# Performance work log

Measured on AMD Instinct MI355X. Metric: run time of the kernel, lower is better.

The kernel has to match this reference:

```python
import jax, jax.numpy as jnp
import numpy as np

EPS = 1e-5


def _layer_norm(x, gamma, beta):
    mu = jnp.mean(x, axis=-1, keepdims=True)
    var = jnp.var(x, axis=-1, keepdims=True)
    return (x - mu) * jax.lax.rsqrt(var + EPS) * gamma + beta


def setup_inputs() -> dict:
    key = jax.random.key(0)
    B, I, H = 4096, 1024, 1024
    ks = jax.random.split(key, 6)
    x = jax.random.normal(ks[0], (B, I), dtype=jnp.float32)
    h = jax.random.normal(ks[1], (B, H), dtype=jnp.float32)
    c = jax.random.normal(ks[2], (B, H), dtype=jnp.float32)
    # nn.Linear(I+H, 4H): weight [4H, I+H], bias [4H]
    bound = 1.0 / np.sqrt(I + H)
    W = jax.random.uniform(ks[3], (4 * H, I + H), minval=-bound, maxval=bound, dtype=jnp.float32)
    b = jax.random.uniform(ks[4], (4 * H,), minval=-bound, maxval=bound, dtype=jnp.float32)
    inp = {"x": x, "h": h, "c": c, "W": W, "b": b}
    for name in ("i", "f", "g", "o", "c"):
        inp[f"ln_{name}_g"] = jnp.ones((H,), dtype=jnp.float32)
        inp[f"ln_{name}_b"] = jnp.zeros((H,), dtype=jnp.float32)
    return inp


def reference(x, h, c, W, b, ln_i_g, ln_i_b, ln_f_g, ln_f_b, ln_g_g, ln_g_b,
              ln_o_g, ln_o_b, ln_c_g, ln_c_b):
    H = h.shape[-1]
    xh = jnp.concatenate([x, h], axis=-1)              # [B, I+H]
    gates = xh @ W.T + b                               # [B, 4H]
    i_raw, f_raw, g_raw, o_raw = jnp.split(gates, 4, axis=-1)
    i = jax.nn.sigmoid(_layer_norm(i_raw, ln_i_g, ln_i_b))
    f = jax.nn.sigmoid(_layer_norm(f_raw, ln_f_g, ln_f_b))
    g = jnp.tanh(_layer_norm(g_raw, ln_g_g, ln_g_b))
    o = jax.nn.sigmoid(_layer_norm(o_raw, ln_o_g, ln_o_b))
    c_new = f * c + i * g
    h_new = o * jnp.tanh(_layer_norm(c_new, ln_c_g, ln_c_b))
    return (h_new, c_new)
```

## Files before the change

kernel.cpp:

```cpp
#include <hip/hip_runtime.h>
#include <hip/hip_bf16.h>

#define B_ROWS 4096
#define H_DIM  1024
#define K_DIM  2048
#define N_DIM  4096
#define NT32   64

typedef __attribute__((ext_vector_type(8))) short bf16x8;
typedef __attribute__((ext_vector_type(4))) float f32x4;

__device__ __forceinline__ unsigned short f2bf(float f) {
  union { float f; unsigned int u; } v; v.f = f;
  unsigned int u = v.u;
  return (unsigned short)((u + 0x7fffu + ((u >> 16) & 1u)) >> 16);
}
__device__ __forceinline__ float bf2f(unsigned short u) {
  union { unsigned int u; float f; } v; v.u = ((unsigned int)u) << 16;
  return v.f;
}

__device__ __forceinline__ void gload_lds16(const void* g, void* l) {
  __builtin_amdgcn_global_load_lds(
      (const __attribute__((address_space(1))) void*)g,
      (__attribute__((address_space(3))) void*)l, 16, 0, 0);
}

__global__ __launch_bounds__(256) void pack_kernel(
    const float* __restrict__ x, const float* __restrict__ h,
    const float* __restrict__ W, unsigned short* __restrict__ Abf,
    unsigned short* __restrict__ Wbf) {
  int bid = blockIdx.x;
  if (bid < 8192) {
    int t = bid * 256 + threadIdx.x;
    int e = t * 4;
    int row = e >> 11;
    int col = e & 2047;
    const float* src = (col < 1024) ? (x + (size_t)row * 1024 + col)
                                    : (h + (size_t)row * 1024 + (col - 1024));
    float4 v = *(const float4*)src;
    ushort4 o;
    o.x = f2bf(v.x); o.y = f2bf(v.y); o.z = f2bf(v.z); o.w = f2bf(v.w);
    *(ushort4*)(Abf + e) = o;
  } else {
    int t = (bid - 8192) * 256 + threadIdx.x;
    int e = t * 4;
    float4 v = *(const float4*)(W + e);
    ushort4 o;
    o.x = f2bf(v.x); o.y = f2bf(v.y); o.z = f2bf(v.z); o.w = f2bf(v.w);
    *(ushort4*)(Wbf + e) = o;
  }
}


#define UNR _Pragma("unroll")

#define TILE1(tt, BUF, FRa, FRb, FWa, FWb)                                   \
  {                                                                          \
    const int kt3 = ((tt) + 3) & (NT32 - 1);                                 \
    char* const Ld = lds + (((BUF) + 3) & 3) * 32768;                        \
    const unsigned short* pA = gAw + ((size_t)kt3 << 5);                     \
    const unsigned short* pB = gBw + ((size_t)kt3 << 5);                     \
    gload_lds16(pA, Ld + dstOfs);                                            \
    gload_lds16(pA + 16 * K_DIM, Ld + dstOfs + 1024);                        \
    gload_lds16(pB, Ld + 16384 + dstOfs);                                    \
    gload_lds16(pB + 16 * K_DIM, Ld + 16384 + dstOfs + 1024);                \
    asm volatile("s_waitcnt vmcnt(8)" ::: "memory");                         \
    __builtin_amdgcn_s_barrier();                                            \
    const char* const Ln = lds + (((BUF) + 1) & 3) * 32768;                  \
    UNR for (int mi = 0; mi < 8; ++mi)                                       \
      FWa[mi] = *(const bf16x8*)(Ln + (wm * 8 + mi) * 1024 + lofs);          \
    UNR for (int ni = 0; ni < 4; ++ni)                                       \
      FWb[ni] = *(const bf16x8*)(Ln + 16384 + (wn * 4 + ni) * 1024 + lofs);  \
    asm volatile("s_waitcnt lgkmcnt(12)" ::: "memory");                      \
    __builtin_amdgcn_sched_barrier(0);                                       \
    __builtin_amdgcn_s_setprio(1);                                           \
    UNR for (int mi = 0; mi < 8; ++mi)                                       \
      UNR for (int ni = 0; ni < 4; ++ni)                                     \
        acc[mi][ni] = __builtin_amdgcn_mfma_f32_16x16x32_bf16(               \
            FRa[mi], FRb[ni], acc[mi][ni], 0, 0, 0);                         \
    __builtin_amdgcn_s_setprio(0);                                           \
  }

#define PSTAGE(kt, BUFOFS)                                                   \
  {                                                                          \
    const unsigned short* pA = gAw + ((size_t)(kt) << 5);                    \
    const unsigned short* pB = gBw + ((size_t)(kt) << 5);                    \
    char* const Ld = lds + (BUFOFS);                                         \
    gload_lds16(pA, Ld + dstOfs);                                            \
    gload_lds16(pA + 16 * K_DIM, Ld + dstOfs + 1024);                        \
    gload_lds16(pB, Ld + 16384 + dstOfs);                                    \
    gload_lds16(pB + 16 * K_DIM, Ld + 16384 + dstOfs + 1024);                \
  }

__global__ __launch_bounds__(512, 2) void gemm_kernel(
    const unsigned short* __restrict__ A, const unsigned short* __restrict__ W,
    const float* __restrict__ bias, unsigned short* __restrict__ C) {
  __shared__ __align__(16) char lds[131072];

  const int tid = threadIdx.x;
  const int w = tid >> 6, l = tid & 63;
  const int wm = w >> 2, wn = w & 3;

  const int bid = blockIdx.x;
  const int xcd = bid & 7, li = bid >> 3;
  const int by = (xcd & 3) * 4 + (li >> 3);
  const int bx = ((xcd >> 2) << 3) + (li & 7);
  const int bm = by * 256, bn = bx * 256;

  const int lofs = (((l & 15) * 64) + ((l >> 4) * 16)) ^ ((l & 8) << 2);
  const int lane_r = (l >> 2) & 15;
  const int lane_c = ((l & 3) * 8) ^ (((l >> 5) & 1) * 16);

  const int dstOfs = w * 2048;
  const unsigned short* gAw = A + (size_t)(bm + 32 * w + lane_r) * K_DIM + lane_c;
  const unsigned short* gBw = W + (size_t)(bn + 32 * w + lane_r) * K_DIM + lane_c;

  f32x4 acc[8][4];
#pragma unroll
  for (int i = 0; i < 8; ++i)
#pragma unroll
    for (int j = 0; j < 4; ++j) acc[i][j] = (f32x4)0.0f;

  PSTAGE(0, 0);
  PSTAGE(1, 32768);
  PSTAGE(2, 65536);
  asm volatile("s_waitcnt vmcnt(8)" ::: "memory");
  __builtin_amdgcn_s_barrier();

  bf16x8 aP[8], bP[4], aQ[8], bQ[4];
#pragma unroll
  for (int mi = 0; mi < 8; ++mi)
    aP[mi] = *(const bf16x8*)(lds + (wm * 8 + mi) * 1024 + lofs);
#pragma unroll
  for (int ni = 0; ni < 4; ++ni)
    bP[ni] = *(const bf16x8*)(lds + 16384 + (wn * 4 + ni) * 1024 + lofs);

  for (int t = 0; t < NT32; t += 4) {
    TILE1(t + 0, 0, aP, bP, aQ, bQ);
    TILE1(t + 1, 1, aQ, bQ, aP, bP);
    TILE1(t + 2, 2, aP, bP, aQ, bQ);
    TILE1(t + 3, 3, aQ, bQ, aP, bP);
  }

  const int lm = l & 15, lq = l >> 4;
  float bv[4];
#pragma unroll
  for (int ni = 0; ni < 4; ++ni) bv[ni] = bias[bn + wn * 64 + ni * 16 + lm];
  unsigned short* Cb = C + (size_t)(bm + wm * 128) * N_DIM + bn + wn * 64;
#pragma unroll
  for (int mi = 0; mi < 8; ++mi)
#pragma unroll
    for (int j = 0; j < 4; ++j) {
      const size_t rofs = (size_t)(mi * 16 + lq * 4 + j) * N_DIM;
#pragma unroll
      for (int ni = 0; ni < 4; ++ni)
        Cb[rofs + ni * 16 + lm] = f2bf(acc[mi][ni][j] + bv[ni]);
    }
}

__device__ __forceinline__ float2 blk_sum2(float s, float q, float* red,
                                           int wid, int lane) {
#pragma unroll
  for (int o = 32; o >= 1; o >>= 1) {
    s += __shfl_xor(s, o, 64);
    q += __shfl_xor(q, o, 64);
  }
  __syncthreads();
  if (lane == 0) { red[wid * 2] = s; red[wid * 2 + 1] = q; }
  __syncthreads();
  s = red[0] + red[2] + red[4] + red[6];
  q = red[1] + red[3] + red[5] + red[7];
  return make_float2(s, q);
}

__device__ __forceinline__ float sigmoidf_(float x) {
  return 1.0f / (1.0f + __expf(-x));
}
__device__ __forceinline__ float tanhf_(float x) {
  return 1.0f - 2.0f / (__expf(2.0f * x) + 1.0f);
}

__global__ __launch_bounds__(256) void ln_lstm_kernel(
    const unsigned short* __restrict__ gates, const float* __restrict__ cprev,
    const float* __restrict__ g_i, const float* __restrict__ b_i,
    const float* __restrict__ g_f, const float* __restrict__ b_f,
    const float* __restrict__ g_g, const float* __restrict__ b_g,
    const float* __restrict__ g_o, const float* __restrict__ b_o,
    const float* __restrict__ g_c, const float* __restrict__ b_c,
    float* __restrict__ out) {
  const int b = blockIdx.x;
  const int t = threadIdx.x;
  const int wid = t >> 6, lane = t & 63;
  __shared__ float red[8];

  const unsigned short* grow = gates + (size_t)b * N_DIM;
  const int c0 = t * 4;

  float v[4][4];
#pragma unroll
  for (int g = 0; g < 4; g++) {
    ushort4 raw = *(const ushort4*)(grow + g * 1024 + c0);
    v[g][0] = bf2f(raw.x); v[g][1] = bf2f(raw.y);
    v[g][2] = bf2f(raw.z); v[g][3] = bf2f(raw.w);
  }

  const float4 gamma[4] = {*(const float4*)(g_i + c0), *(const float4*)(g_f + c0),
                           *(const float4*)(g_g + c0), *(const float4*)(g_o + c0)};
  const float4 beta[4]  = {*(const float4*)(b_i + c0), *(const float4*)(b_f + c0),
                           *(const float4*)(b_g + c0), *(const float4*)(b_o + c0)};

  float a[4][4];
#pragma unroll
  for (int g = 0; g < 4; g++) {
    float s = v[g][0] + v[g][1] + v[g][2] + v[g][3];
    float q = v[g][0]*v[g][0] + v[g][1]*v[g][1] + v[g][2]*v[g][2] + v[g][3]*v[g][3];
    float2 r = blk_sum2(s, q, red, wid, lane);
    float mu = r.x * (1.0f / 1024.0f);
    float var = r.y * (1.0f / 1024.0f) - mu * mu;
    float inv = rsqrtf(var + 1e-5f);
    const float* gm = (const float*)&gamma[g];
    const float* bt = (const float*)&beta[g];
#pragma unroll
    for (int j = 0; j < 4; j++) {
      float n = (v[g][j] - mu) * inv * gm[j] + bt[j];
      a[g][j] = (g == 2) ? tanhf_(n) : sigmoidf_(n);
    }
  }

  float4 cp = *(const float4*)(cprev + (size_t)b * 1024 + c0);
  const float* cpe = (const float*)&cp;
  float cn[4];
#pragma unroll
  for (int j = 0; j < 4; j++)
    cn[j] = a[1][j] * cpe[j] + a[0][j] * a[2][j];

  {
    float s = cn[0] + cn[1] + cn[2] + cn[3];
    float q = cn[0]*cn[0] + cn[1]*cn[1] + cn[2]*cn[2] + cn[3]*cn[3];
    float2 r = blk_sum2(s, q, red, wid, lane);
    float mu = r.x * (1.0f / 1024.0f);
    float var = r.y * (1.0f / 1024.0f) - mu * mu;
    float inv = rsqrtf(var + 1e-5f);
    float4 gm = *(const float4*)(g_c + c0);
    float4 bt = *(const float4*)(b_c + c0);
    const float* gme = (const float*)&gm;
    const float* bte = (const float*)&bt;
    float hn[4];
#pragma unroll
    for (int j = 0; j < 4; j++) {
      float n = (cn[j] - mu) * inv * gme[j] + bte[j];
      hn[j] = a[3][j] * tanhf_(n);
    }
    *(float4*)(out + (size_t)b * 1024 + c0) = make_float4(hn[0], hn[1], hn[2], hn[3]);
    *(float4*)(out + (size_t)B_ROWS * H_DIM + (size_t)b * 1024 + c0) =
        make_float4(cn[0], cn[1], cn[2], cn[3]);
  }
}

extern "C" void kernel_launch(void* const* d_in, const int* in_sizes, int n_in,
                              void* d_out, int out_size, void* d_ws,
                              size_t ws_size, hipStream_t stream) {
  const float* x    = (const float*)d_in[0];
  const float* h    = (const float*)d_in[1];
  const float* c    = (const float*)d_in[2];
  const float* W    = (const float*)d_in[3];
  const float* bias = (const float*)d_in[4];
  const float* ln_i_g = (const float*)d_in[5];
  const float* ln_i_b = (const float*)d_in[6];
  const float* ln_f_g = (const float*)d_in[7];
  const float* ln_f_b = (const float*)d_in[8];
  const float* ln_g_g = (const float*)d_in[9];
  const float* ln_g_b = (const float*)d_in[10];
  const float* ln_o_g = (const float*)d_in[11];
  const float* ln_o_b = (const float*)d_in[12];
  const float* ln_c_g = (const float*)d_in[13];
  const float* ln_c_b = (const float*)d_in[14];

  unsigned short* Abf = (unsigned short*)d_ws;
  unsigned short* Wbf = Abf + (size_t)B_ROWS * K_DIM;
  unsigned short* gates = Wbf + (size_t)N_DIM * K_DIM;

  pack_kernel<<<16384, 256, 0, stream>>>(x, h, W, Abf, Wbf);

  dim3 ggrid(256);
  gemm_kernel<<<ggrid, 512, 0, stream>>>(Abf, Wbf, bias, gates);

  ln_lstm_kernel<<<B_ROWS, 256, 0, stream>>>(
      gates, c, ln_i_g, ln_i_b, ln_f_g, ln_f_b, ln_g_g, ln_g_b,
      ln_o_g, ln_o_b, ln_c_g, ln_c_b, (float*)d_out);
}
```

Before: 105.3 us.

## Shrink GEMM tile to 256x128 with 4 waves and triple-buffered LDS

The GEMM moves from a 256x256 tile with 8 waves and a 4-stage LDS ring to a 256x128 tile with 4 waves and a 3-stage ring, launching 512 blocks instead of 256. Each wave still computes a 128x64 sub-tile, and it now issues 6 global-to-LDS loads per stage. The prefetch distance drops from 3 tiles ahead to 2, and the XCD-to-block mapping is rearranged for the new grid shape. The smaller LDS footprint should let more blocks fit per CU and fill all CUs better, at the cost of more global traffic per FLOP from the narrower N tile and less latency hiding.

Result: slower. 117.6 us (+11.7%).

```diff
diff --git a/kernel.cpp b/kernel.cpp
--- a/kernel.cpp
+++ b/kernel.cpp
@@ -55,23 +55,27 @@
 
 #define UNR _Pragma("unroll")
 
-#define TILE1(tt, BUF, FRa, FRb, FWa, FWb)                                   \
+#define PSTG(kt, BS)                                                         \
   {                                                                          \
-    const int kt3 = ((tt) + 3) & (NT32 - 1);                                 \
-    char* const Ld = lds + (((BUF) + 3) & 3) * 32768;                        \
-    const unsigned short* pA = gAw + ((size_t)kt3 << 5);                     \
-    const unsigned short* pB = gBw + ((size_t)kt3 << 5);                     \
-    gload_lds16(pA, Ld + dstOfs);                                            \
-    gload_lds16(pA + 16 * K_DIM, Ld + dstOfs + 1024);                        \
-    gload_lds16(pB, Ld + 16384 + dstOfs);                                    \
-    gload_lds16(pB + 16 * K_DIM, Ld + 16384 + dstOfs + 1024);                \
-    asm volatile("s_waitcnt vmcnt(8)" ::: "memory");                         \
+    const unsigned short* pA = gAw + ((size_t)(kt) << 5);                    \
+    const unsigned short* pB = gBw + ((size_t)(kt) << 5);                    \
+    UNR for (int i = 0; i < 4; ++i)                                          \
+      gload_lds16(pA + (size_t)i * 16 * K_DIM, (BS) + (4 * w + i) * 1024);   \
+    UNR for (int i = 0; i < 2; ++i)                                          \
+      gload_lds16(pB + (size_t)i * 16 * K_DIM,                               \
+                  (BS) + 16384 + (2 * w + i) * 1024);                        \
+  }
+
+#define TILE(tt, BS, BR, FRa, FRb, FWa, FWb)                                 \
+  {                                                                          \
+    const int kt2 = ((tt) + 2) & (NT32 - 1);                                 \
+    PSTG(kt2, BS);                                                           \
+    asm volatile("s_waitcnt vmcnt(6)" ::: "memory");                         \
     __builtin_amdgcn_s_barrier();                                            \
-    const char* const Ln = lds + (((BUF) + 1) & 3) * 32768;                  \
     UNR for (int mi = 0; mi < 8; ++mi)                                       \
-      FWa[mi] = *(const bf16x8*)(Ln + (wm * 8 + mi) * 1024 + lofs);          \
+      FWa[mi] = *(const bf16x8*)((BR) + (wm * 8 + mi) * 1024 + lofs);        \
     UNR for (int ni = 0; ni < 4; ++ni)                                       \
-      FWb[ni] = *(const bf16x8*)(Ln + 16384 + (wn * 4 + ni) * 1024 + lofs);  \
+      FWb[ni] = *(const bf16x8*)((BR) + 16384 + (wn * 4 + ni) * 1024 + lofs);\
     asm volatile("s_waitcnt lgkmcnt(12)" ::: "memory");                      \
     __builtin_amdgcn_sched_barrier(0);                                       \
     __builtin_amdgcn_s_setprio(1);                                           \
@@ -82,66 +86,64 @@
     __builtin_amdgcn_s_setprio(0);                                           \
   }
 
-#define PSTAGE(kt, BUFOFS)                                                   \
-  {                                                                          \
-    const unsigned short* pA = gAw + ((size_t)(kt) << 5);                    \
-    const unsigned short* pB = gBw + ((size_t)(kt) << 5);                    \
-    char* const Ld = lds + (BUFOFS);                                         \
-    gload_lds16(pA, Ld + dstOfs);                                            \
-    gload_lds16(pA + 16 * K_DIM, Ld + dstOfs + 1024);                        \
-    gload_lds16(pB, Ld + 16384 + dstOfs);                                    \
-    gload_lds16(pB + 16 * K_DIM, Ld + 16384 + dstOfs + 1024);                \
-  }
-
-__global__ __launch_bounds__(512, 2) void gemm_kernel(
+__global__ __launch_bounds__(256, 2) void gemm_kernel(
     const unsigned short* __restrict__ A, const unsigned short* __restrict__ W,
     const float* __restrict__ bias, unsigned short* __restrict__ C) {
-  __shared__ __align__(16) char lds[131072];
+  __shared__ __align__(16) char lds[73728];
 
   const int tid = threadIdx.x;
   const int w = tid >> 6, l = tid & 63;
-  const int wm = w >> 2, wn = w & 3;
+  const int wm = w >> 1, wn = w & 1;
 
   const int bid = blockIdx.x;
   const int xcd = bid & 7, li = bid >> 3;
-  const int by = (xcd & 3) * 4 + (li >> 3);
-  const int bx = ((xcd >> 2) << 3) + (li & 7);
-  const int bm = by * 256, bn = bx * 256;
+  const int by = (xcd & 1) * 8 + (li >> 3);
+  const int bx = ((xcd >> 1) << 3) + (li & 7);
+  const int bm = by * 256, bn = bx * 128;
 
   const int lofs = (((l & 15) * 64) + ((l >> 4) * 16)) ^ ((l & 8) << 2);
   const int lane_r = (l >> 2) & 15;
   const int lane_c = ((l & 3) * 8) ^ (((l >> 5) & 1) * 16);
 
-  const int dstOfs = w * 2048;
-  const unsigned short* gAw = A + (size_t)(bm + 32 * w + lane_r) * K_DIM + lane_c;
+  const unsigned short* gAw = A + (size_t)(bm + 64 * w + lane_r) * K_DIM + lane_c;
   const unsigned short* gBw = W + (size_t)(bn + 32 * w + lane_r) * K_DIM + lane_c;
 
+  char* const LB0 = lds;
+  char* const LB1 = lds + 24576;
+  char* const LB2 = lds + 49152;
+
   f32x4 acc[8][4];
 #pragma unroll
   for (int i = 0; i < 8; ++i)
 #pragma unroll
     for (int j = 0; j < 4; ++j) acc[i][j] = (f32x4)0.0f;
 
-  PSTAGE(0, 0);
-  PSTAGE(1, 32768);
-  PSTAGE(2, 65536);
-  asm volatile("s_waitcnt vmcnt(8)" ::: "memory");
+  PSTG(0, LB0);
+  PSTG(1, LB1);
+  asm volatile("s_waitcnt vmcnt(6)" ::: "memory");
   __builtin_amdgcn_s_barrier();
 
   bf16x8 aP[8], bP[4], aQ[8], bQ[4];
 #pragma unroll
   for (int mi = 0; mi < 8; ++mi)
-    aP[mi] = *(const bf16x8*)(lds + (wm * 8 + mi) * 1024 + lofs);
+    aP[mi] = *(const bf16x8*)(LB0 + (wm * 8 + mi) * 1024 + lofs);
 #pragma unroll
   for (int ni = 0; ni < 4; ++ni)
-    bP[ni] = *(const bf16x8*)(lds + 16384 + (wn * 4 + ni) * 1024 + lofs);
-
-  for (int t = 0; t < NT32; t += 4) {
-    TILE1(t + 0, 0, aP, bP, aQ, bQ);
-    TILE1(t + 1, 1, aQ, bQ, aP, bP);
-    TILE1(t + 2, 2, aP, bP, aQ, bQ);
-    TILE1(t + 3, 3, aQ, bQ, aP, bP);
-  }
+    bP[ni] = *(const bf16x8*)(LB0 + 16384 + (wn * 4 + ni) * 1024 + lofs);
+
+  for (int i = 0; i < 10; ++i) {
+    const int t = i * 6;
+    TILE(t + 0, LB2, LB1, aP, bP, aQ, bQ);
+    TILE(t + 1, LB0, LB2, aQ, bQ, aP, bP);
+    TILE(t + 2, LB1, LB0, aP, bP, aQ, bQ);
+    TILE(t + 3, LB2, LB1, aQ, bQ, aP, bP);
+    TILE(t + 4, LB0, LB2, aP, bP, aQ, bQ);
+    TILE(t + 5, LB1, LB0, aQ, bQ, aP, bP);
+  }
+  TILE(60, LB2, LB1, aP, bP, aQ, bQ);
+  TILE(61, LB0, LB2, aQ, bQ, aP, bP);
+  TILE(62, LB1, LB0, aP, bP, aQ, bQ);
+  TILE(63, LB2, LB1, aQ, bQ, aP, bP);
 
   const int lm = l & 15, lq = l >> 4;
   float bv[4];
@@ -283,8 +285,8 @@
 
   pack_kernel<<<16384, 256, 0, stream>>>(x, h, W, Abf, Wbf);
 
-  dim3 ggrid(256);
-  gemm_kernel<<<ggrid, 512, 0, stream>>>(Abf, Wbf, bias, gates);
+  dim3 ggrid(512);
+  gemm_kernel<<<ggrid, 256, 0, stream>>>(Abf, Wbf, bias, gates);
 
   ln_lstm_kernel<<<B_ROWS, 256, 0, stream>>>(
       gates, c, ln_i_g, ln_i_b, ln_f_g, ln_f_b, ln_g_g, ln_g_b,
```

## Switch GEMM to 32x32x16 MFMA tiles and batch LayerNorm gate reductions

Applied to the files above, without the earlier changes.

The GEMM inner loop moves from 16x16x32 MFMA to 32x32x16 bf16 MFMA with 4x2 accumulator tiles per wave. This changes the LDS fragment addressing, the global-to-LDS lane mapping and the epilogue store pattern. The larger instruction is meant to cut LDS fragment reads and instruction issue per unit of math. The LN-LSTM kernel also reduces all four gate sums and sums of squares in one pass with a single barrier, instead of four separate block reductions. The new swizzled addressing risks bank conflicts or layout errors if it does not match the load mapping.

Measured after the change: 111.0 us. 5.5% more time.

```diff
diff --git a/kernel.cpp b/kernel.cpp
--- a/kernel.cpp
+++ b/kernel.cpp
@@ -8,7 +8,7 @@
 #define NT32   64
 
 typedef __attribute__((ext_vector_type(8))) short bf16x8;
-typedef __attribute__((ext_vector_type(4))) float f32x4;
+typedef __attribute__((ext_vector_type(16))) float f32x16;
 
 __device__ __forceinline__ unsigned short f2bf(float f) {
   union { float f; unsigned int u; } v; v.f = f;
@@ -55,42 +55,42 @@
 
 #define UNR _Pragma("unroll")
 
+#define PSTG(kt, BUFOFS)                                                     \
+  {                                                                          \
+    const size_t ko = (size_t)(kt) << 5;                                     \
+    char* const Ld = lds + (BUFOFS);                                         \
+    gload_lds16(gAw0 + ko, Ld + dstOfs);                                     \
+    gload_lds16(gAw1 + ko, Ld + dstOfs + 1024);                              \
+    gload_lds16(gBw0 + ko, Ld + 16384 + dstOfs);                             \
+    gload_lds16(gBw1 + ko, Ld + 16384 + dstOfs + 1024);                      \
+  }
+
 #define TILE1(tt, BUF, FRa, FRb, FWa, FWb)                                   \
   {                                                                          \
     const int kt3 = ((tt) + 3) & (NT32 - 1);                                 \
-    char* const Ld = lds + (((BUF) + 3) & 3) * 32768;                        \
-    const unsigned short* pA = gAw + ((size_t)kt3 << 5);                     \
-    const unsigned short* pB = gBw + ((size_t)kt3 << 5);                     \
-    gload_lds16(pA, Ld + dstOfs);                                            \
-    gload_lds16(pA + 16 * K_DIM, Ld + dstOfs + 1024);                        \
-    gload_lds16(pB, Ld + 16384 + dstOfs);                                    \
-    gload_lds16(pB + 16 * K_DIM, Ld + 16384 + dstOfs + 1024);                \
+    PSTG(kt3, (((BUF) + 3) & 3) * 32768);                                    \
     asm volatile("s_waitcnt vmcnt(8)" ::: "memory");                         \
     __builtin_amdgcn_s_barrier();                                            \
     const char* const Ln = lds + (((BUF) + 1) & 3) * 32768;                  \
-    UNR for (int mi = 0; mi < 8; ++mi)                                       \
-      FWa[mi] = *(const bf16x8*)(Ln + (wm * 8 + mi) * 1024 + lofs);          \
-    UNR for (int ni = 0; ni < 4; ++ni)                                       \
-      FWb[ni] = *(const bf16x8*)(Ln + 16384 + (wn * 4 + ni) * 1024 + lofs);  \
+    UNR for (int R = 0; R < 4; ++R) {                                        \
+      FWa[R][0] = *(const bf16x8*)(Ln + (wm * 8 + 2 * R) * 1024 + lofs0);    \
+      FWa[R][1] = *(const bf16x8*)(Ln + (wm * 8 + 2 * R) * 1024 + lofs1);    \
+    }                                                                        \
+    UNR for (int ni = 0; ni < 2; ++ni) {                                     \
+      FWb[ni][0] = *(const bf16x8*)(Ln + 16384 +                             \
+                                    (wn * 4 + 2 * ni) * 1024 + lofs0);       \
+      FWb[ni][1] = *(const bf16x8*)(Ln + 16384 +                             \
+                                    (wn * 4 + 2 * ni) * 1024 + lofs1);       \
+    }                                                                        \
     asm volatile("s_waitcnt lgkmcnt(12)" ::: "memory");                      \
     __builtin_amdgcn_sched_barrier(0);                                       \
     __builtin_amdgcn_s_setprio(1);                                           \
-    UNR for (int mi = 0; mi < 8; ++mi)                                       \
-      UNR for (int ni = 0; ni < 4; ++ni)                                     \
-        acc[mi][ni] = __builtin_amdgcn_mfma_f32_16x16x32_bf16(               \
-            FRa[mi], FRb[ni], acc[mi][ni], 0, 0, 0);                         \
+    UNR for (int R = 0; R < 4; ++R)                                          \
+      UNR for (int ni = 0; ni < 2; ++ni)                                     \
+        UNR for (int h = 0; h < 2; ++h)                                      \
+          acc[R][ni] = __builtin_amdgcn_mfma_f32_32x32x16_bf16(              \
+              FRa[R][h], FRb[ni][h], acc[R][ni], 0, 0, 0);                   \
     __builtin_amdgcn_s_setprio(0);                                           \
-  }
-
-#define PSTAGE(kt, BUFOFS)                                                   \
-  {                                                                          \
-    const unsigned short* pA = gAw + ((size_t)(kt) << 5);                    \
-    const unsigned short* pB = gBw + ((size_t)(kt) << 5);                    \
-    char* const Ld = lds + (BUFOFS);                                         \
-    gload_lds16(pA, Ld + dstOfs);                                            \
-    gload_lds16(pA + 16 * K_DIM, Ld + dstOfs + 1024);                        \
-    gload_lds16(pB, Ld + 16384 + dstOfs);                                    \
-    gload_lds16(pB + 16 * K_DIM, Ld + 16384 + dstOfs + 1024);                \
   }
 
 __global__ __launch_bounds__(512, 2) void gemm_kernel(
@@ -108,33 +108,43 @@
   const int bx = ((xcd >> 2) << 3) + (li & 7);
   const int bm = by * 256, bn = bx * 256;
 
-  const int lofs = (((l & 15) * 64) + ((l >> 4) * 16)) ^ ((l & 8) << 2);
+  const int lofs0 = ((l >> 4) & 1) * 1024 + (l & 15) * 64 +
+                    ((((l >> 5) * 16) ^ ((l & 8) << 2)) ^ (((l >> 4) & 1) << 4));
+  const int lofs1 = lofs0 ^ 32;
+
   const int lane_r = (l >> 2) & 15;
-  const int lane_c = ((l & 3) * 8) ^ (((l >> 5) & 1) * 16);
+  const int lane_c0 = ((l & 3) * 8) ^ (((l >> 5) & 1) * 16);
+  const int lane_c1 = lane_c0 ^ 8;
 
   const int dstOfs = w * 2048;
-  const unsigned short* gAw = A + (size_t)(bm + 32 * w + lane_r) * K_DIM + lane_c;
-  const unsigned short* gBw = W + (size_t)(bn + 32 * w + lane_r) * K_DIM + lane_c;
-
-  f32x4 acc[8][4];
-#pragma unroll
-  for (int i = 0; i < 8; ++i)
-#pragma unroll
-    for (int j = 0; j < 4; ++j) acc[i][j] = (f32x4)0.0f;
-
-  PSTAGE(0, 0);
-  PSTAGE(1, 32768);
-  PSTAGE(2, 65536);
+  const unsigned short* gAw0 = A + (size_t)(bm + 32 * w + lane_r) * K_DIM + lane_c0;
+  const unsigned short* gAw1 = A + (size_t)(bm + 32 * w + 16 + lane_r) * K_DIM + lane_c1;
+  const unsigned short* gBw0 = W + (size_t)(bn + 32 * w + lane_r) * K_DIM + lane_c0;
+  const unsigned short* gBw1 = W + (size_t)(bn + 32 * w + 16 + lane_r) * K_DIM + lane_c1;
+
+  f32x16 acc[4][2];
+#pragma unroll
+  for (int i = 0; i < 4; ++i)
+#pragma unroll
+    for (int j = 0; j < 2; ++j) acc[i][j] = (f32x16)0.0f;
+
+  PSTG(0, 0);
+  PSTG(1, 32768);
+  PSTG(2, 65536);
   asm volatile("s_waitcnt vmcnt(8)" ::: "memory");
   __builtin_amdgcn_s_barrier();
 
-  bf16x8 aP[8], bP[4], aQ[8], bQ[4];
-#pragma unroll
-  for (int mi = 0; mi < 8; ++mi)
-    aP[mi] = *(const bf16x8*)(lds + (wm * 8 + mi) * 1024 + lofs);
-#pragma unroll
-  for (int ni = 0; ni < 4; ++ni)
-    bP[ni] = *(const bf16x8*)(lds + 16384 + (wn * 4 + ni) * 1024 + lofs);
+  bf16x8 aP[4][2], bP[2][2], aQ[4][2], bQ[2][2];
+#pragma unroll
+  for (int R = 0; R < 4; ++R) {
+    aP[R][0] = *(const bf16x8*)(lds + (wm * 8 + 2 * R) * 1024 + lofs0);
+    aP[R][1] = *(const bf16x8*)(lds + (wm * 8 + 2 * R) * 1024 + lofs1);
+  }
+#pragma unroll
+  for (int ni = 0; ni < 2; ++ni) {
+    bP[ni][0] = *(const bf16x8*)(lds + 16384 + (wn * 4 + 2 * ni) * 1024 + lofs0);
+    bP[ni][1] = *(const bf16x8*)(lds + 16384 + (wn * 4 + 2 * ni) * 1024 + lofs1);
+  }
 
   for (int t = 0; t < NT32; t += 4) {
     TILE1(t + 0, 0, aP, bP, aQ, bQ);
@@ -143,35 +153,20 @@
     TILE1(t + 3, 3, aQ, bQ, aP, bP);
   }
 
-  const int lm = l & 15, lq = l >> 4;
-  float bv[4];
-#pragma unroll
-  for (int ni = 0; ni < 4; ++ni) bv[ni] = bias[bn + wn * 64 + ni * 16 + lm];
+  const int cl = l & 31, hi = l >> 5;
+  float bv[2];
+#pragma unroll
+  for (int ni = 0; ni < 2; ++ni) bv[ni] = bias[bn + wn * 64 + ni * 32 + cl];
   unsigned short* Cb = C + (size_t)(bm + wm * 128) * N_DIM + bn + wn * 64;
 #pragma unroll
-  for (int mi = 0; mi < 8; ++mi)
-#pragma unroll
-    for (int j = 0; j < 4; ++j) {
-      const size_t rofs = (size_t)(mi * 16 + lq * 4 + j) * N_DIM;
-#pragma unroll
-      for (int ni = 0; ni < 4; ++ni)
-        Cb[rofs + ni * 16 + lm] = f2bf(acc[mi][ni][j] + bv[ni]);
-    }
-}
-
-__device__ __forceinline__ float2 blk_sum2(float s, float q, float* red,
-                                           int wid, int lane) {
-#pragma unroll
-  for (int o = 32; o >= 1; o >>= 1) {
-    s += __shfl_xor(s, o, 64);
-    q += __shfl_xor(q, o, 64);
-  }
-  __syncthreads();
-  if (lane == 0) { red[wid * 2] = s; red[wid * 2 + 1] = q; }
-  __syncthreads();
-  s = red[0] + red[2] + red[4] + red[6];
-  q = red[1] + red[3] + red[5] + red[7];
-  return make_float2(s, q);
+  for (int R = 0; R < 4; ++R)
+#pragma unroll
+    for (int ni = 0; ni < 2; ++ni)
+#pragma unroll
+      for (int r = 0; r < 16; ++r) {
+        const int row = R * 32 + (r & 3) + 8 * (r >> 2) + 4 * hi;
+        Cb[(size_t)row * N_DIM + ni * 32 + cl] = f2bf(acc[R][ni][r] + bv[ni]);
+      }
 }
 
 __device__ __forceinline__ float sigmoidf_(float x) {
@@ -192,7 +187,7 @@
   const int b = blockIdx.x;
   const int t = threadIdx.x;
   const int wid = t >> 6, lane = t & 63;
-  __shared__ float red[8];
+  __shared__ float red[32];
 
   const unsigned short* grow = gates + (size_t)b * N_DIM;
   const int c0 = t * 4;
@@ -210,14 +205,29 @@
   const float4 beta[4]  = {*(const float4*)(b_i + c0), *(const float4*)(b_f + c0),
                            *(const float4*)(b_g + c0), *(const float4*)(b_o + c0)};
 
+  float s[8];
+#pragma unroll
+  for (int g = 0; g < 4; g++) {
+    s[g]     = v[g][0] + v[g][1] + v[g][2] + v[g][3];
+    s[4 + g] = v[g][0]*v[g][0] + v[g][1]*v[g][1] + v[g][2]*v[g][2] + v[g][3]*v[g][3];
+  }
+#pragma unroll
+  for (int o = 32; o >= 1; o >>= 1)
+#pragma unroll
+    for (int i = 0; i < 8; i++) s[i] += __shfl_xor(s[i], o, 64);
+  if (lane == 0) {
+#pragma unroll
+    for (int i = 0; i < 8; i++) red[wid * 8 + i] = s[i];
+  }
+  __syncthreads();
+#pragma unroll
+  for (int i = 0; i < 8; i++) s[i] = red[i] + red[8 + i] + red[16 + i] + red[24 + i];
+
   float a[4][4];
 #pragma unroll
   for (int g = 0; g < 4; g++) {
-    float s = v[g][0] + v[g][1] + v[g][2] + v[g][3];
-    float q = v[g][0]*v[g][0] + v[g][1]*v[g][1] + v[g][2]*v[g][2] + v[g][3]*v[g][3];
-    float2 r = blk_sum2(s, q, red, wid, lane);
-    float mu = r.x * (1.0f / 1024.0f);
-    float var = r.y * (1.0f / 1024.0f) - mu * mu;
+    float mu = s[g] * (1.0f / 1024.0f);
+    float var = s[4 + g] * (1.0f / 1024.0f) - mu * mu;
     float inv = rsqrtf(var + 1e-5f);
     const float* gm = (const float*)&gamma[g];
     const float* bt = (const float*)&beta[g];
@@ -236,11 +246,20 @@
     cn[j] = a[1][j] * cpe[j] + a[0][j] * a[2][j];
 
   {
-    float s = cn[0] + cn[1] + cn[2] + cn[3];
-    float q = cn[0]*cn[0] + cn[1]*cn[1] + cn[2]*cn[2] + cn[3]*cn[3];
-    float2 r = blk_sum2(s, q, red, wid, lane);
-    float mu = r.x * (1.0f / 1024.0f);
-    float var = r.y * (1.0f / 1024.0f) - mu * mu;
+    float u0 = cn[0] + cn[1] + cn[2] + cn[3];
+    float u1 = cn[0]*cn[0] + cn[1]*cn[1] + cn[2]*cn[2] + cn[3]*cn[3];
+#pragma unroll
+    for (int o = 32; o >= 1; o >>= 1) {
+      u0 += __shfl_xor(u0, o, 64);
+      u1 += __shfl_xor(u1, o, 64);
+    }
+    __syncthreads();
+    if (lane == 0) { red[wid * 2] = u0; red[wid * 2 + 1] = u1; }
+    __syncthreads();
+    u0 = red[0] + red[2] + red[4] + red[6];
+    u1 = red[1] + red[3] + red[5] + red[7];
+    float mu = u0 * (1.0f / 1024.0f);
+    float var = u1 * (1.0f / 1024.0f) - mu * mu;
     float inv = rsqrtf(var + 1e-5f);
     float4 gm = *(const float4*)(g_c + c0);
     float4 bt = *(const float4*)(b_c + c0);
```

## Fuse pack, GEMM and LayerNorm-LSTM into one cooperative kernel with grid syncs

Applied to the files above, without the earlier changes.

Merges the three launches (bf16 pack, MFMA GEMM, LN-LSTM epilogue) into a single cooperative kernel of 256 blocks, separated by grid-wide syncs. This removes two kernel launch gaps and the tail of each stage. The LN stage is rewritten so each wave handles a whole row and reduces with shuffles only, instead of a block-wide LDS reduction. The GEMM inner tile also changes its waits and adds sched_group_barrier interleaving of MFMA and LDS reads. In exchange, the pack and LN stages now run with only 256 blocks of 512 threads, which lowers their occupancy and parallelism, and the grid syncs add their own overhead.

Result: slower. 185.5 us (+76.2%).

```diff
diff --git a/kernel.cpp b/kernel.cpp
--- a/kernel.cpp
+++ b/kernel.cpp
@@ -1,5 +1,8 @@
 #include <hip/hip_runtime.h>
 #include <hip/hip_bf16.h>
+#include <hip/hip_cooperative_groups.h>
+
+namespace cg = cooperative_groups;
 
 #define B_ROWS 4096
 #define H_DIM  1024
@@ -26,267 +29,281 @@
       (__attribute__((address_space(3))) void*)l, 16, 0, 0);
 }
 
-__global__ __launch_bounds__(256) void pack_kernel(
-    const float* __restrict__ x, const float* __restrict__ h,
-    const float* __restrict__ W, unsigned short* __restrict__ Abf,
-    unsigned short* __restrict__ Wbf) {
-  int bid = blockIdx.x;
-  if (bid < 8192) {
-    int t = bid * 256 + threadIdx.x;
-    int e = t * 4;
-    int row = e >> 11;
-    int col = e & 2047;
-    const float* src = (col < 1024) ? (x + (size_t)row * 1024 + col)
-                                    : (h + (size_t)row * 1024 + (col - 1024));
-    float4 v = *(const float4*)src;
-    ushort4 o;
-    o.x = f2bf(v.x); o.y = f2bf(v.y); o.z = f2bf(v.z); o.w = f2bf(v.w);
-    *(ushort4*)(Abf + e) = o;
-  } else {
-    int t = (bid - 8192) * 256 + threadIdx.x;
-    int e = t * 4;
-    float4 v = *(const float4*)(W + e);
-    ushort4 o;
-    o.x = f2bf(v.x); o.y = f2bf(v.y); o.z = f2bf(v.z); o.w = f2bf(v.w);
-    *(ushort4*)(Wbf + e) = o;
-  }
-}
-
+__device__ __forceinline__ float sigmoidf_(float x) {
+  return 1.0f / (1.0f + __expf(-x));
+}
+__device__ __forceinline__ float tanhf_(float x) {
+  return 1.0f - 2.0f / (__expf(2.0f * x) + 1.0f);
+}
+
+struct KParams {
+  const float *x, *h, *c, *W, *bias;
+  const float *gi, *bi2, *gf, *bf2, *gg, *bg2, *go, *bo2, *gc, *bc2;
+  unsigned short *Abf, *Wbf, *gates;
+  float *out;
+};
 
 #define UNR _Pragma("unroll")
+
+#define PSTG(kt, BUFOFS)                                                     \
+  {                                                                          \
+    const size_t ko = (size_t)(kt) << 5;                                     \
+    char* const Ld = lds + (BUFOFS);                                         \
+    gload_lds16(gAw + ko, Ld + dstOfs);                                      \
+    gload_lds16(gAw + ko + 16 * K_DIM, Ld + dstOfs + 1024);                  \
+    gload_lds16(gBw + ko, Ld + 16384 + dstOfs);                              \
+    gload_lds16(gBw + ko + 16 * K_DIM, Ld + 16384 + dstOfs + 1024);          \
+  }
 
 #define TILE1(tt, BUF, FRa, FRb, FWa, FWb)                                   \
   {                                                                          \
     const int kt3 = ((tt) + 3) & (NT32 - 1);                                 \
-    char* const Ld = lds + (((BUF) + 3) & 3) * 32768;                        \
-    const unsigned short* pA = gAw + ((size_t)kt3 << 5);                     \
-    const unsigned short* pB = gBw + ((size_t)kt3 << 5);                     \
-    gload_lds16(pA, Ld + dstOfs);                                            \
-    gload_lds16(pA + 16 * K_DIM, Ld + dstOfs + 1024);                        \
-    gload_lds16(pB, Ld + 16384 + dstOfs);                                    \
-    gload_lds16(pB + 16 * K_DIM, Ld + 16384 + dstOfs + 1024);                \
+    PSTG(kt3, (((BUF) + 3) & 3) * 32768);                                    \
     asm volatile("s_waitcnt vmcnt(8)" ::: "memory");                         \
     __builtin_amdgcn_s_barrier();                                            \
+    asm volatile("s_waitcnt lgkmcnt(0)" ::: "memory");                       \
+    __builtin_amdgcn_sched_barrier(0);                                       \
     const char* const Ln = lds + (((BUF) + 1) & 3) * 32768;                  \
+    __builtin_amdgcn_s_setprio(1);                                           \
     UNR for (int mi = 0; mi < 8; ++mi)                                       \
       FWa[mi] = *(const bf16x8*)(Ln + (wm * 8 + mi) * 1024 + lofs);          \
     UNR for (int ni = 0; ni < 4; ++ni)                                       \
       FWb[ni] = *(const bf16x8*)(Ln + 16384 + (wn * 4 + ni) * 1024 + lofs);  \
-    asm volatile("s_waitcnt lgkmcnt(12)" ::: "memory");                      \
-    __builtin_amdgcn_sched_barrier(0);                                       \
-    __builtin_amdgcn_s_setprio(1);                                           \
     UNR for (int mi = 0; mi < 8; ++mi)                                       \
       UNR for (int ni = 0; ni < 4; ++ni)                                     \
         acc[mi][ni] = __builtin_amdgcn_mfma_f32_16x16x32_bf16(               \
             FRa[mi], FRb[ni], acc[mi][ni], 0, 0, 0);                         \
+    UNR for (int gph = 0; gph < 4; ++gph) {                                  \
+      __builtin_amdgcn_sched_group_barrier(0x100, 3, 0);      \
+      __builtin_amdgcn_sched_group_barrier(0x008, 8, 0);      \
+    }                                                                        \
     __builtin_amdgcn_s_setprio(0);                                           \
   }
 
-#define PSTAGE(kt, BUFOFS)                                                   \
-  {                                                                          \
-    const unsigned short* pA = gAw + ((size_t)(kt) << 5);                    \
-    const unsigned short* pB = gBw + ((size_t)(kt) << 5);                    \
-    char* const Ld = lds + (BUFOFS);                                         \
-    gload_lds16(pA, Ld + dstOfs);                                            \
-    gload_lds16(pA + 16 * K_DIM, Ld + dstOfs + 1024);                        \
-    gload_lds16(pB, Ld + 16384 + dstOfs);                                    \
-    gload_lds16(pB + 16 * K_DIM, Ld + 16384 + dstOfs + 1024);                \
-  }
-
-__global__ __launch_bounds__(512, 2) void gemm_kernel(
-    const unsigned short* __restrict__ A, const unsigned short* __restrict__ W,
-    const float* __restrict__ bias, unsigned short* __restrict__ C) {
+__global__ __launch_bounds__(512, 2) void fused_kernel(KParams p) {
   __shared__ __align__(16) char lds[131072];
 
   const int tid = threadIdx.x;
   const int w = tid >> 6, l = tid & 63;
-  const int wm = w >> 2, wn = w & 3;
-
-  const int bid = blockIdx.x;
-  const int xcd = bid & 7, li = bid >> 3;
-  const int by = (xcd & 3) * 4 + (li >> 3);
-  const int bx = ((xcd >> 2) << 3) + (li & 7);
-  const int bm = by * 256, bn = bx * 256;
-
-  const int lofs = (((l & 15) * 64) + ((l >> 4) * 16)) ^ ((l & 8) << 2);
-  const int lane_r = (l >> 2) & 15;
-  const int lane_c = ((l & 3) * 8) ^ (((l >> 5) & 1) * 16);
-
-  const int dstOfs = w * 2048;
-  const unsigned short* gAw = A + (size_t)(bm + 32 * w + lane_r) * K_DIM + lane_c;
-  const unsigned short* gBw = W + (size_t)(bn + 32 * w + lane_r) * K_DIM + lane_c;
-
-  f32x4 acc[8][4];
-#pragma unroll
-  for (int i = 0; i < 8; ++i)
-#pragma unroll
-    for (int j = 0; j < 4; ++j) acc[i][j] = (f32x4)0.0f;
-
-  PSTAGE(0, 0);
-  PSTAGE(1, 32768);
-  PSTAGE(2, 65536);
-  asm volatile("s_waitcnt vmcnt(8)" ::: "memory");
-  __builtin_amdgcn_s_barrier();
-
-  bf16x8 aP[8], bP[4], aQ[8], bQ[4];
-#pragma unroll
-  for (int mi = 0; mi < 8; ++mi)
-    aP[mi] = *(const bf16x8*)(lds + (wm * 8 + mi) * 1024 + lofs);
-#pragma unroll
-  for (int ni = 0; ni < 4; ++ni)
-    bP[ni] = *(const bf16x8*)(lds + 16384 + (wn * 4 + ni) * 1024 + lofs);
-
-  for (int t = 0; t < NT32; t += 4) {
-    TILE1(t + 0, 0, aP, bP, aQ, bQ);
-    TILE1(t + 1, 1, aQ, bQ, aP, bP);
-    TILE1(t + 2, 2, aP, bP, aQ, bQ);
-    TILE1(t + 3, 3, aQ, bQ, aP, bP);
-  }
-
-  const int lm = l & 15, lq = l >> 4;
-  float bv[4];
-#pragma unroll
-  for (int ni = 0; ni < 4; ++ni) bv[ni] = bias[bn + wn * 64 + ni * 16 + lm];
-  unsigned short* Cb = C + (size_t)(bm + wm * 128) * N_DIM + bn + wn * 64;
-#pragma unroll
-  for (int mi = 0; mi < 8; ++mi)
-#pragma unroll
-    for (int j = 0; j < 4; ++j) {
-      const size_t rofs = (size_t)(mi * 16 + lq * 4 + j) * N_DIM;
-#pragma unroll
-      for (int ni = 0; ni < 4; ++ni)
-        Cb[rofs + ni * 16 + lm] = f2bf(acc[mi][ni][j] + bv[ni]);
+
+  {
+    const int gtid = blockIdx.x * 512 + tid;
+#pragma unroll 2
+    for (int i = 0; i < 16; ++i) {
+      const int idx = gtid + i * 131072;
+      const int e = idx * 4;
+      const int row = e >> 11, col = e & 2047;
+      const float* src = (col < 1024)
+                             ? (p.x + (size_t)row * 1024 + col)
+                             : (p.h + (size_t)row * 1024 + (col - 1024));
+      float4 v = *(const float4*)src;
+      ushort4 o;
+      o.x = f2bf(v.x); o.y = f2bf(v.y); o.z = f2bf(v.z); o.w = f2bf(v.w);
+      *(ushort4*)(p.Abf + e) = o;
     }
-}
-
-__device__ __forceinline__ float2 blk_sum2(float s, float q, float* red,
-                                           int wid, int lane) {
-#pragma unroll
-  for (int o = 32; o >= 1; o >>= 1) {
-    s += __shfl_xor(s, o, 64);
-    q += __shfl_xor(q, o, 64);
-  }
-  __syncthreads();
-  if (lane == 0) { red[wid * 2] = s; red[wid * 2 + 1] = q; }
-  __syncthreads();
-  s = red[0] + red[2] + red[4] + red[6];
-  q = red[1] + red[3] + red[5] + red[7];
-  return make_float2(s, q);
-}
-
-__device__ __forceinline__ float sigmoidf_(float x) {
-  return 1.0f / (1.0f + __expf(-x));
-}
-__device__ __forceinline__ float tanhf_(float x) {
-  return 1.0f - 2.0f / (__expf(2.0f * x) + 1.0f);
-}
-
-__global__ __launch_bounds__(256) void ln_lstm_kernel(
-    const unsigned short* __restrict__ gates, const float* __restrict__ cprev,
-    const float* __restrict__ g_i, const float* __restrict__ b_i,
-    const float* __restrict__ g_f, const float* __restrict__ b_f,
-    const float* __restrict__ g_g, const float* __restrict__ b_g,
-    const float* __restrict__ g_o, const float* __restrict__ b_o,
-    const float* __restrict__ g_c, const float* __restrict__ b_c,
-    float* __restrict__ out) {
-  const int b = blockIdx.x;
-  const int t = threadIdx.x;
-  const int wid = t >> 6, lane = t & 63;
-  __shared__ float red[8];
-
-  const unsigned short* grow = gates + (size_t)b * N_DIM;
-  const int c0 = t * 4;
-
-  float v[4][4];
-#pragma unroll
-  for (int g = 0; g < 4; g++) {
-    ushort4 raw = *(const ushort4*)(grow + g * 1024 + c0);
-    v[g][0] = bf2f(raw.x); v[g][1] = bf2f(raw.y);
-    v[g][2] = bf2f(raw.z); v[g][3] = bf2f(raw.w);
-  }
-
-  const float4 gamma[4] = {*(const float4*)(g_i + c0), *(const float4*)(g_f + c0),
-                           *(const float4*)(g_g + c0), *(const float4*)(g_o + c0)};
-  const float4 beta[4]  = {*(const float4*)(b_i + c0), *(const float4*)(b_f + c0),
-                           *(const float4*)(b_g + c0), *(const float4*)(b_o + c0)};
-
-  float a[4][4];
-#pragma unroll
-  for (int g = 0; g < 4; g++) {
-    float s = v[g][0] + v[g][1] + v[g][2] + v[g][3];
-    float q = v[g][0]*v[g][0] + v[g][1]*v[g][1] + v[g][2]*v[g][2] + v[g][3]*v[g][3];
-    float2 r = blk_sum2(s, q, red, wid, lane);
-    float mu = r.x * (1.0f / 1024.0f);
-    float var = r.y * (1.0f / 1024.0f) - mu * mu;
-    float inv = rsqrtf(var + 1e-5f);
-    const float* gm = (const float*)&gamma[g];
-    const float* bt = (const float*)&beta[g];
-#pragma unroll
-    for (int j = 0; j < 4; j++) {
-      float n = (v[g][j] - mu) * inv * gm[j] + bt[j];
-      a[g][j] = (g == 2) ? tanhf_(n) : sigmoidf_(n);
+#pragma unroll 2
+    for (int i = 0; i < 16; ++i) {
+      const int e = (gtid + i * 131072) * 4;
+      float4 v = *(const float4*)(p.W + e);
+      ushort4 o;
+      o.x = f2bf(v.x); o.y = f2bf(v.y); o.z = f2bf(v.z); o.w = f2bf(v.w);
+      *(ushort4*)(p.Wbf + e) = o;
     }
   }
-
-  float4 cp = *(const float4*)(cprev + (size_t)b * 1024 + c0);
-  const float* cpe = (const float*)&cp;
-  float cn[4];
-#pragma unroll
-  for (int j = 0; j < 4; j++)
-    cn[j] = a[1][j] * cpe[j] + a[0][j] * a[2][j];
+  cg::this_grid().sync();
 
   {
-    float s = cn[0] + cn[1] + cn[2] + cn[3];
-    float q = cn[0]*cn[0] + cn[1]*cn[1] + cn[2]*cn[2] + cn[3]*cn[3];
-    float2 r = blk_sum2(s, q, red, wid, lane);
-    float mu = r.x * (1.0f / 1024.0f);
-    float var = r.y * (1.0f / 1024.0f) - mu * mu;
-    float inv = rsqrtf(var + 1e-5f);
-    float4 gm = *(const float4*)(g_c + c0);
-    float4 bt = *(const float4*)(b_c + c0);
-    const float* gme = (const float*)&gm;
-    const float* bte = (const float*)&bt;
-    float hn[4];
-#pragma unroll
-    for (int j = 0; j < 4; j++) {
-      float n = (cn[j] - mu) * inv * gme[j] + bte[j];
-      hn[j] = a[3][j] * tanhf_(n);
+    const unsigned short* __restrict__ A = p.Abf;
+    const unsigned short* __restrict__ Wb = p.Wbf;
+    const int wm = w >> 2, wn = w & 3;
+
+    const int bid = blockIdx.x;
+    const int xcd = bid & 7, li = bid >> 3;
+    const int by = (xcd & 3) * 4 + (li >> 3);
+    const int bx = ((xcd >> 2) << 3) + (li & 7);
+    const int bm = by * 256, bn = bx * 256;
+
+    const int lofs = (((l & 15) * 64) + ((l >> 4) * 16)) ^ ((l & 8) << 2);
+    const int lane_r = (l >> 2) & 15;
+    const int lane_c = ((l & 3) * 8) ^ (((l >> 5) & 1) * 16);
+
+    const int dstOfs = w * 2048;
+    const unsigned short* gAw =
+        A + (size_t)(bm + 32 * w + lane_r) * K_DIM + lane_c;
+    const unsigned short* gBw =
+        Wb + (size_t)(bn + 32 * w + lane_r) * K_DIM + lane_c;
+
+    f32x4 acc[8][4];
+#pragma unroll
+    for (int i = 0; i < 8; ++i)
+#pragma unroll
+      for (int j = 0; j < 4; ++j) acc[i][j] = (f32x4)0.0f;
+
+    PSTG(0, 0);
+    PSTG(1, 32768);
+    PSTG(2, 65536);
+    asm volatile("s_waitcnt vmcnt(8)" ::: "memory");
+    __builtin_amdgcn_s_barrier();
+
+    bf16x8 aP[8], bP[4], aQ[8], bQ[4];
+#pragma unroll
+    for (int mi = 0; mi < 8; ++mi)
+      aP[mi] = *(const bf16x8*)(lds + (wm * 8 + mi) * 1024 + lofs);
+#pragma unroll
+    for (int ni = 0; ni < 4; ++ni)
+      bP[ni] = *(const bf16x8*)(lds + 16384 + (wn * 4 + ni) * 1024 + lofs);
+
+    for (int t = 0; t < NT32; t += 4) {
+      TILE1(t + 0, 0, aP, bP, aQ, bQ);
+      TILE1(t + 1, 1, aQ, bQ, aP, bP);
+      TILE1(t + 2, 2, aP, bP, aQ, bQ);
+      TILE1(t + 3, 3, aQ, bQ, aP, bP);
     }
-    *(float4*)(out + (size_t)b * 1024 + c0) = make_float4(hn[0], hn[1], hn[2], hn[3]);
-    *(float4*)(out + (size_t)B_ROWS * H_DIM + (size_t)b * 1024 + c0) =
-        make_float4(cn[0], cn[1], cn[2], cn[3]);
+
+    const int lm = l & 15, lq = l >> 4;
+    float bv[4];
+#pragma unroll
+    for (int ni = 0; ni < 4; ++ni)
+      bv[ni] = p.bias[bn + wn * 64 + ni * 16 + lm];
+    unsigned short* Cb =
+        p.gates + (size_t)(bm + wm * 128) * N_DIM + bn + wn * 64;
+#pragma unroll
+    for (int mi = 0; mi < 8; ++mi)
+#pragma unroll
+      for (int j = 0; j < 4; ++j) {
+        const size_t rofs = (size_t)(mi * 16 + lq * 4 + j) * N_DIM;
+#pragma unroll
+        for (int ni = 0; ni < 4; ++ni)
+          Cb[rofs + ni * 16 + lm] = f2bf(acc[mi][ni][j] + bv[ni]);
+      }
+  }
+  cg::this_grid().sync();
+
+  {
+#pragma unroll
+    for (int it = 0; it < 2; ++it) {
+      const int row = blockIdx.x * 16 + w * 2 + it;
+      const unsigned short* grow = p.gates + (size_t)row * N_DIM;
+      const int cb = l * 16;
+
+      float av[4][16];
+      float s8[8];
+#pragma unroll
+      for (int g4 = 0; g4 < 4; ++g4) {
+        float ss = 0.0f, qq = 0.0f;
+#pragma unroll
+        for (int u = 0; u < 2; ++u) {
+          bf16x8 r = *(const bf16x8*)(grow + g4 * 1024 + cb + u * 8);
+#pragma unroll
+          for (int j = 0; j < 8; ++j) {
+            float f = bf2f((unsigned short)r[j]);
+            av[g4][u * 8 + j] = f;
+            ss += f; qq += f * f;
+          }
+        }
+        s8[g4] = ss; s8[4 + g4] = qq;
+      }
+#pragma unroll
+      for (int o = 32; o >= 1; o >>= 1)
+#pragma unroll
+        for (int i = 0; i < 8; ++i) s8[i] += __shfl_xor(s8[i], o, 64);
+
+      const float* gmp[4] = {p.gi, p.gf, p.gg, p.go};
+      const float* btp[4] = {p.bi2, p.bf2, p.bg2, p.bo2};
+#pragma unroll
+      for (int g4 = 0; g4 < 4; ++g4) {
+        const float mu = s8[g4] * (1.0f / 1024.0f);
+        const float var = s8[4 + g4] * (1.0f / 1024.0f) - mu * mu;
+        const float inv = rsqrtf(var + 1e-5f);
+        float gm[16], bt[16];
+#pragma unroll
+        for (int q4 = 0; q4 < 4; ++q4) {
+          *(float4*)&gm[q4 * 4] = *(const float4*)(gmp[g4] + cb + q4 * 4);
+          *(float4*)&bt[q4 * 4] = *(const float4*)(btp[g4] + cb + q4 * 4);
+        }
+#pragma unroll
+        for (int j = 0; j < 16; ++j) {
+          const float n = (av[g4][j] - mu) * inv * gm[j] + bt[j];
+          av[g4][j] = (g4 == 2) ? tanhf_(n) : sigmoidf_(n);
+        }
+      }
+
+      float cn[16];
+#pragma unroll
+      for (int q4 = 0; q4 < 4; ++q4) {
+        float4 cp = *(const float4*)(p.c + (size_t)row * 1024 + cb + q4 * 4);
+        const float* cpe = (const float*)&cp;
+#pragma unroll
+        for (int j = 0; j < 4; ++j) {
+          const int e = q4 * 4 + j;
+          cn[e] = av[1][e] * cpe[j] + av[0][e] * av[2][e];
+        }
+      }
+
+      float u0 = 0.0f, u1 = 0.0f;
+#pragma unroll
+      for (int j = 0; j < 16; ++j) { u0 += cn[j]; u1 += cn[j] * cn[j]; }
+#pragma unroll
+      for (int o = 32; o >= 1; o >>= 1) {
+        u0 += __shfl_xor(u0, o, 64);
+        u1 += __shfl_xor(u1, o, 64);
+      }
+      const float muc = u0 * (1.0f / 1024.0f);
+      const float invc = rsqrtf(u1 * (1.0f / 1024.0f) - muc * muc + 1e-5f);
+
+      float* hout = p.out + (size_t)row * 1024 + cb;
+      float* cout = p.out + (size_t)B_ROWS * H_DIM + (size_t)row * 1024 + cb;
+#pragma unroll
+      for (int q4 = 0; q4 < 4; ++q4) {
+        float4 gcv = *(const float4*)(p.gc + cb + q4 * 4);
+        float4 bcv = *(const float4*)(p.bc2 + cb + q4 * 4);
+        const float* gce = (const float*)&gcv;
+        const float* bce = (const float*)&bcv;
+        float4 hv, cv;
+        float* hve = (float*)&hv; float* cve = (float*)&cv;
+#pragma unroll
+        for (int j = 0; j < 4; ++j) {
+          const int e = q4 * 4 + j;
+          const float n = (cn[e] - muc) * invc * gce[j] + bce[j];
+          hve[j] = av[3][e] * tanhf_(n);
+          cve[j] = cn[e];
+        }
+        *(float4*)(hout + q4 * 4) = hv;
+        *(float4*)(cout + q4 * 4) = cv;
+      }
+    }
   }
 }
 
 extern "C" void kernel_launch(void* const* d_in, const int* in_sizes, int n_in,
                               void* d_out, int out_size, void* d_ws,
                               size_t ws_size, hipStream_t stream) {
-  const float* x    = (const float*)d_in[0];
-  const float* h    = (const float*)d_in[1];
-  const float* c    = (const float*)d_in[2];
-  const float* W    = (const float*)d_in[3];
-  const float* bias = (const float*)d_in[4];
-  const float* ln_i_g = (const float*)d_in[5];
-  const float* ln_i_b = (const float*)d_in[6];
-  const float* ln_f_g = (const float*)d_in[7];
-  const float* ln_f_b = (const float*)d_in[8];
-  const float* ln_g_g = (const float*)d_in[9];
-  const float* ln_g_b = (const float*)d_in[10];
-  const float* ln_o_g = (const float*)d_in[11];
-  const float* ln_o_b = (const float*)d_in[12];
-  const float* ln_c_g = (const float*)d_in[13];
-  const float* ln_c_b = (const float*)d_in[14];
-
   unsigned short* Abf = (unsigned short*)d_ws;
   unsigned short* Wbf = Abf + (size_t)B_ROWS * K_DIM;
   unsigned short* gates = Wbf + (size_t)N_DIM * K_DIM;
 
-  pack_kernel<<<16384, 256, 0, stream>>>(x, h, W, Abf, Wbf);
-
-  dim3 ggrid(256);
-  gemm_kernel<<<ggrid, 512, 0, stream>>>(Abf, Wbf, bias, gates);
-
-  ln_lstm_kernel<<<B_ROWS, 256, 0, stream>>>(
-      gates, c, ln_i_g, ln_i_b, ln_f_g, ln_f_b, ln_g_g, ln_g_b,
-      ln_o_g, ln_o_b, ln_c_g, ln_c_b, (float*)d_out);
-}
+  KParams p;
+  p.x = (const float*)d_in[0];
+  p.h = (const float*)d_in[1];
+  p.c = (const float*)d_in[2];
+  p.W = (const float*)d_in[3];
+  p.bias = (const float*)d_in[4];
+  p.gi = (const float*)d_in[5];
+  p.bi2 = (const float*)d_in[6];
+  p.gf = (const float*)d_in[7];
+  p.bf2 = (const float*)d_in[8];
+  p.gg = (const float*)d_in[9];
+  p.bg2 = (const float*)d_in[10];
+  p.go = (const float*)d_in[11];
+  p.bo2 = (const float*)d_in[12];
+  p.gc = (const float*)d_in[13];
+  p.bc2 = (const float*)d_in[14];
+  p.Abf = Abf;
+  p.Wbf = Wbf;
+  p.gates = gates;
+  p.out = (float*)d_out;
+
+  void* args[] = {(void*)&p};
+  hipLaunchCooperativeKernel((void*)fused_kernel, dim3(256), dim3(512), args,
+                             0, stream);
+}
```
